# Performance work log

Measured on AMD Instinct MI355X. Metric: run time of the kernel, lower is better.

The kernel has to match this reference:

```python
import jax, jax.numpy as jnp
import numpy as np

RADIUS = 2
B, C, D, H, W = 2, 16, 48, 128, 256
G = 3 * (2 * RADIUS + 1) ** 2  # 75 guidance channels: (2r+1)^2 spatial x 3 depth offsets


def setup_inputs() -> dict:
    key = jax.random.key(0)
    k1, k2 = jax.random.split(key)
    input1 = jax.random.normal(k1, (B, C, D, H, W), dtype=jnp.float32)  # cost volume
    input2 = jax.random.normal(k2, (B, G, H, W), dtype=jnp.float32) * 0.1  # guidance weights
    return {"input1": input1, "input2": input2}


def _lga3d(x, g, r):
    """One pass of local guided aggregation.
    x: [B,C,D,H,W] cost volume; g: [B, 3*(2r+1)^2, H, W] per-pixel weights.
    out[b,c,d,h,w] = sum_{i,j in (2r+1)^2 window, k in {d-1,d,d+1}}
                     g[b, (i*(2r+1)+j)*3+k, h, w] * x[b,c,d+k-1,h+i-r,w+j-r]
    (zero padding out of bounds; weights shared across channels)."""
    w = 2 * r + 1
    bb, cc, dd, hh, ww = x.shape
    # pad depth by 1 on each side, spatial by r on each side
    xp = jnp.pad(x, ((0, 0), (0, 0), (1, 1), (r, r), (r, r)))
    out = jnp.zeros_like(x)
    for i in range(w):          # fixed small window loop (not a data-dim loop)
        for j in range(w):
            for k in range(3):  # depth offsets -1, 0, +1
                idx = (i * w + j) * 3 + k
                patch = jax.lax.dynamic_slice(xp, (0, 0, k, i, j), (bb, cc, dd, hh, ww))
                out = out + g[:, idx][:, None, None, :, :] * patch
    return out


def reference(input1, input2):
    # '2' in LGA3D2: aggregation applied twice with the same guidance
    y = _lga3d(input1, input2, RADIUS)
    return _lga3d(y, input2, RADIUS)
```

## Files before the change

### kernel.cpp

```cpp
#include <hip/hip_runtime.h>
#include <hip/hip_bf16.h>


constexpr int RAD = 2;
constexpr int BB = 2, CC = 16, DD = 48, HH = 128, WW = 256;
constexpr int GG = 75;
constexpr int PLANE = HH * WW;

constexpr int WPT = 4;
constexpr int DPG = 6;
constexpr int NWV = 4;
constexpr int DCHUNK = DPG * NWV;
constexpr int NCH = DD / DCHUNK;
constexpr size_t GPB_UINTS = (size_t)BB * 5 * 9 * PLANE;

using uint = unsigned int;
typedef __attribute__((ext_vector_type(2))) _Float16 half2v;

__device__ __forceinline__ uint pkrtz(float a, float b) {
  return __builtin_bit_cast(uint, __builtin_amdgcn_cvt_pkrtz(a, b));
}
__device__ __forceinline__ float fdot2(uint a, uint b, float c) {
#if __has_builtin(__builtin_amdgcn_fdot2)
  return __builtin_amdgcn_fdot2(__builtin_bit_cast(half2v, a),
                                __builtin_bit_cast(half2v, b), c, false);
#else
  half2v av = __builtin_bit_cast(half2v, a), bv = __builtin_bit_cast(half2v, b);
  return c + (float)av.x * (float)bv.x + (float)av.y * (float)bv.y;
#endif
}
__device__ __forceinline__ uint alignp(uint a, uint b) {
  return __builtin_amdgcn_alignbit(a, b, 16);
}
__device__ __forceinline__ unsigned short f2h(float v) {
  return __builtin_bit_cast(unsigned short, (_Float16)v);
}
__device__ __forceinline__ uint getq(const uint4& v, int q) {
  return q == 0 ? v.x : q == 1 ? v.y : q == 2 ? v.z : v.w;
}

__global__ __launch_bounds__(256) void cvt_f32_f16(const float* __restrict__ x,
                                                   unsigned short* __restrict__ xh,
                                                   int n4) {
  const int stride = gridDim.x * blockDim.x;
  for (int i = blockIdx.x * blockDim.x + threadIdx.x; i < n4; i += stride) {
    const float4 v = *reinterpret_cast<const float4*>(x + (size_t)i * 4);
    uint2 u; u.x = pkrtz(v.x, v.y); u.y = pkrtz(v.z, v.w);
    *reinterpret_cast<uint2*>(xh + (size_t)i * 4) = u;
  }
}

__global__ __launch_bounds__(256) void gpack(const float* __restrict__ g,
                                             uint4* __restrict__ gbuf) {
  const int n = (int)(GPB_UINTS / 4);
  const int stride = gridDim.x * blockDim.x;
  for (int it = blockIdx.x * blockDim.x + threadIdx.x; it < n; it += stride) {
    const int p  = it % 9;
    const int wq = (it / 9) & 63;
    const int h  = (it / (9 * 64)) % HH;
    const int bi = it / (9 * 64 * HH);
    const int i = bi % 5, b = bi / 5;
    const int k = p / 3, jp = p % 3;
    const int chA = (i * 5 + 2 * jp) * 3 + k;
    const float* gb = g + (size_t)b * GG * PLANE + h * WW + 4 * wq;
    const float4 a = *reinterpret_cast<const float4*>(gb + (size_t)chA * PLANE);
    float4 bq = make_float4(0.f, 0.f, 0.f, 0.f);
    if (jp < 2)
      bq = *reinterpret_cast<const float4*>(gb + (size_t)(chA + 3) * PLANE);
    uint4 u;
    u.x = pkrtz(a.x, bq.x); u.y = pkrtz(a.y, bq.y);
    u.z = pkrtz(a.z, bq.z); u.w = pkrtz(a.w, bq.w);
    gbuf[it] = u;
  }
}

template <typename OT, bool PACKED>
__global__ __launch_bounds__(256, 1) void lga_pass(const unsigned short* __restrict__ x,
                                                   const float* __restrict__ g,
                                                   const uint4* __restrict__ gpk,
                                                   OT* __restrict__ out) {
  constexpr int NWG = BB * CC * NCH * HH;
  const int bx = blockIdx.x;
  const int lid = (bx & 7) * (NWG >> 3) + (bx >> 3);
  const int dch = lid % NCH;
  const int h   = (lid / NCH) % HH;
  const int c   = (lid / (NCH * HH)) % CC;
  const int b   =  lid / (NCH * HH * CC);

  const int tid = threadIdx.x;
  const int lane = tid & 63;
  const int dg = tid >> 6;
  const int w0 = lane * WPT;
  const int d0 = dch * DCHUNK + dg * DPG;

  const unsigned short* xb = x + (size_t)(b * CC + c) * DD * PLANE;
  const float* gb = g + (size_t)b * GG * PLANE;

  const int lm1 = ((lane - 1) & 63) * 4;
  const int lp1 = ((lane + 1) & 63) * 4;
  const bool l0 = (lane == 0);
  const bool l63 = (lane == 63);

  float acc[DPG][WPT];
#pragma unroll
  for (int a = 0; a < DPG; ++a)
#pragma unroll
    for (int q = 0; q < WPT; ++q) acc[a][q] = 0.f;

  const int ilo = (h >= RAD) ? 0 : RAD - h;
  const int him = HH - 1 + RAD - h;
  const int ihi = (him < 4) ? him : 4;

  for (int ii = ilo; ii <= ihi; ++ii) {
    const int hr = h + ii - RAD;

    uint4 G[9];
    if constexpr (PACKED) {
      const uint4* gp = gpk + ((size_t)((b * 5 + ii) * HH + h) * 64 + lane) * 9;
#pragma unroll
      for (int p = 0; p < 9; ++p) G[p] = gp[p];
    } else {
#pragma unroll
      for (int k = 0; k < 3; ++k)
#pragma unroll
        for (int jp = 0; jp < 3; ++jp) {
          const int chA = (ii * 5 + 2 * jp) * 3 + k;
          const float4 a = *reinterpret_cast<const float4*>(
              gb + (size_t)chA * PLANE + h * WW + w0);
          float4 bq = make_float4(0.f, 0.f, 0.f, 0.f);
          if (jp < 2)
            bq = *reinterpret_cast<const float4*>(
                gb + (size_t)(chA + 3) * PLANE + h * WW + w0);
          uint4 u;
          u.x = pkrtz(a.x, bq.x); u.y = pkrtz(a.y, bq.y);
          u.z = pkrtz(a.z, bq.z); u.w = pkrtz(a.w, bq.w);
          G[k * 3 + jp] = u;
        }
    }

#pragma unroll
    for (int a = -1; a <= DPG; ++a) {
      bool dok = true;
      if (a == -1)  dok = (d0 > 0);
      if (a == DPG) dok = (d0 + DPG < DD);

      uint2 own = make_uint2(0u, 0u);
      if (dok)
        own = *reinterpret_cast<const uint2*>(
            xb + (size_t)(d0 + a) * PLANE + hr * WW + w0);

      const uint lft = __builtin_amdgcn_ds_bpermute(lm1, (int)own.y);
      const uint rg0 = __builtin_amdgcn_ds_bpermute(lp1, (int)own.x);
      const uint rg1 = __builtin_amdgcn_ds_bpermute(lp1, (int)own.y);
      uint P[9];
      P[0] = l0 ? 0u : lft;
      P[2] = own.x; P[4] = own.y;
      P[6] = l63 ? 0u : rg0;
      P[8] = l63 ? 0u : rg1;
      P[1] = alignp(P[2], P[0]);
      P[3] = alignp(P[4], P[2]);
      P[5] = alignp(P[6], P[4]);
      P[7] = alignp(P[8], P[6]);

#pragma unroll
      for (int k = 0; k < 3; ++k) {
        const int ai = a + 1 - k;
        if (ai < 0 || ai >= DPG) continue;
#pragma unroll
        for (int q = 0; q < WPT; ++q) {
          float t = acc[ai][q];
          t = fdot2(getq(G[k * 3 + 0], q), P[q], t);
          t = fdot2(getq(G[k * 3 + 1], q), P[q + 2], t);
          t = fdot2(getq(G[k * 3 + 2], q), P[q + 4], t);
          acc[ai][q] = t;
        }
      }
    }
  }

  const int obase = d0 * PLANE + h * WW + w0;
  if constexpr (sizeof(OT) == 4) {
    float* ob = (float*)out + (size_t)(b * CC + c) * DD * PLANE;
#pragma unroll
    for (int ai = 0; ai < DPG; ++ai) {
      float4 t; t.x = acc[ai][0]; t.y = acc[ai][1]; t.z = acc[ai][2]; t.w = acc[ai][3];
      *reinterpret_cast<float4*>(ob + obase + ai * PLANE) = t;
    }
  } else {
    unsigned short* ob = (unsigned short*)out + (size_t)(b * CC + c) * DD * PLANE;
#pragma unroll
    for (int ai = 0; ai < DPG; ++ai) {
      ushort4 t; t.x = f2h(acc[ai][0]); t.y = f2h(acc[ai][1]);
      t.z = f2h(acc[ai][2]); t.w = f2h(acc[ai][3]);
      *reinterpret_cast<ushort4*>(ob + obase + ai * PLANE) = t;
    }
  }
}

extern "C" void kernel_launch(void* const* d_in, const int* in_sizes, int n_in,
                              void* d_out, int out_size, void* d_ws, size_t ws_size,
                              hipStream_t stream) {
  const float* x = (const float*)d_in[0];
  const float* g = (const float*)d_in[1];
  float* out = (float*)d_out;

  const size_t elems = (size_t)BB * CC * DD * HH * WW;
  unsigned short* xh = (unsigned short*)d_out;
  unsigned short* y  = (unsigned short*)d_ws;

  cvt_f32_f16<<<2048, 256, 0, stream>>>(x, xh, (int)(elems / 4));

  const dim3 grid(BB * CC * NCH * HH);
  const dim3 block(64 * NWV);

  const size_t need = elems * 2 + GPB_UINTS * 4;
  if (ws_size >= need) {
    uint4* gbuf = (uint4*)((char*)d_ws + elems * 2);
    gpack<<<1440, 256, 0, stream>>>(g, gbuf);
    lga_pass<unsigned short, true><<<grid, block, 0, stream>>>(xh, g, gbuf, y);
    lga_pass<float, true><<<grid, block, 0, stream>>>(y, g, gbuf, out);
  } else {
    lga_pass<unsigned short, false><<<grid, block, 0, stream>>>(xh, g, nullptr, y);
    lga_pass<float, false><<<grid, block, 0, stream>>>(y, g, nullptr, out);
  }
}
```

Measured before the change: 349.6 us.

## Store fp16 volumes in depth/width-padded layout to drop lane shuffles and bounds checks

The fp16 input and intermediate volumes are stored in a padded layout: one zero depth slice on each side and two zero columns left plus six right, giving 264-element rows. Each lane can then load its own 4 columns plus the neighbouring halo with two 8-byte loads. This replaces three ds_bpermute shuffles and the depth-boundary predicates per depth slice. Extra zero_pads kernels write the pads, the conversion and intermediate writes become two 4-byte stores per element group, the buffers grow, and the launch-bounds occupancy hint is relaxed.

```diff
diff --git a/kernel.cpp b/kernel.cpp
--- a/kernel.cpp
+++ b/kernel.cpp
@@ -12,6 +12,10 @@
 constexpr int NWV = 4;
 constexpr int DCHUNK = DPG * NWV;
 constexpr int NCH = DD / DCHUNK;
+constexpr int PW = 264;
+constexpr int DP = DD + 2;
+constexpr size_t PCH = (size_t)DP * HH * PW;
+constexpr size_t PAD_ELEMS = (size_t)BB * CC * PCH;
 constexpr size_t GPB_UINTS = (size_t)BB * 5 * 9 * PLANE;
 
 using uint = unsigned int;
@@ -32,11 +36,23 @@
 __device__ __forceinline__ uint alignp(uint a, uint b) {
   return __builtin_amdgcn_alignbit(a, b, 16);
 }
-__device__ __forceinline__ unsigned short f2h(float v) {
-  return __builtin_bit_cast(unsigned short, (_Float16)v);
-}
 __device__ __forceinline__ uint getq(const uint4& v, int q) {
   return q == 0 ? v.x : q == 1 ? v.y : q == 2 ? v.z : v.w;
+}
+
+__global__ __launch_bounds__(256) void zero_pads(unsigned short* __restrict__ buf) {
+  const int nrows = (int)(BB * CC * DP * HH);
+  const int stride = gridDim.x * blockDim.x;
+  for (int r = blockIdx.x * blockDim.x + threadIdx.x; r < nrows; r += stride) {
+    uint* rowp = reinterpret_cast<uint*>(buf + (size_t)r * PW);
+    const int dpad = (r / HH) % DP;
+    if (dpad == 0 || dpad == DP - 1) {
+      for (int t = 0; t < PW / 2; ++t) rowp[t] = 0u;
+    } else {
+      rowp[0] = 0u;
+      rowp[129] = 0u; rowp[130] = 0u; rowp[131] = 0u;
+    }
+  }
 }
 
 __global__ __launch_bounds__(256) void cvt_f32_f16(const float* __restrict__ x,
@@ -45,8 +61,16 @@
   const int stride = gridDim.x * blockDim.x;
   for (int i = blockIdx.x * blockDim.x + threadIdx.x; i < n4; i += stride) {
     const float4 v = *reinterpret_cast<const float4*>(x + (size_t)i * 4);
-    uint2 u; u.x = pkrtz(v.x, v.y); u.y = pkrtz(v.z, v.w);
-    *reinterpret_cast<uint2*>(xh + (size_t)i * 4) = u;
+    const uint u0 = pkrtz(v.x, v.y);
+    const uint u1 = pkrtz(v.z, v.w);
+    const int w4 = (i & 63) * 4;
+    const int h = (i >> 6) & (HH - 1);
+    const int rest = i >> 13;
+    const int d = rest % DD;
+    const int bc = rest / DD;
+    const size_t hb = ((size_t)(bc * DP + d + 1) * HH + h) * PW + 2 + w4;
+    *reinterpret_cast<uint*>(xh + hb) = u0;
+    *reinterpret_cast<uint*>(xh + hb + 2) = u1;
   }
 }
 
@@ -75,10 +99,10 @@
 }
 
 template <typename OT, bool PACKED>
-__global__ __launch_bounds__(256, 1) void lga_pass(const unsigned short* __restrict__ x,
-                                                   const float* __restrict__ g,
-                                                   const uint4* __restrict__ gpk,
-                                                   OT* __restrict__ out) {
+__global__ __launch_bounds__(256) void lga_pass(const unsigned short* __restrict__ xp,
+                                                const float* __restrict__ g,
+                                                const uint4* __restrict__ gpk,
+                                                OT* __restrict__ out) {
   constexpr int NWG = BB * CC * NCH * HH;
   const int bx = blockIdx.x;
   const int lid = (bx & 7) * (NWG >> 3) + (bx >> 3);
@@ -93,13 +117,9 @@
   const int w0 = lane * WPT;
   const int d0 = dch * DCHUNK + dg * DPG;
 
-  const unsigned short* xb = x + (size_t)(b * CC + c) * DD * PLANE;
+  const int ch = b * CC + c;
+  const unsigned short* xb = xp + (size_t)ch * PCH;
   const float* gb = g + (size_t)b * GG * PLANE;
-
-  const int lm1 = ((lane - 1) & 63) * 4;
-  const int lp1 = ((lane + 1) & 63) * 4;
-  const bool l0 = (lane == 0);
-  const bool l63 = (lane == 63);
 
   float acc[DPG][WPT];
 #pragma unroll
@@ -140,28 +160,15 @@
 
 #pragma unroll
     for (int a = -1; a <= DPG; ++a) {
-      bool dok = true;
-      if (a == -1)  dok = (d0 > 0);
-      if (a == DPG) dok = (d0 + DPG < DD);
-
-      uint2 own = make_uint2(0u, 0u);
-      if (dok)
-        own = *reinterpret_cast<const uint2*>(
-            xb + (size_t)(d0 + a) * PLANE + hr * WW + w0);
-
-      const uint lft = __builtin_amdgcn_ds_bpermute(lm1, (int)own.y);
-      const uint rg0 = __builtin_amdgcn_ds_bpermute(lp1, (int)own.x);
-      const uint rg1 = __builtin_amdgcn_ds_bpermute(lp1, (int)own.y);
-      uint P[9];
-      P[0] = l0 ? 0u : lft;
-      P[2] = own.x; P[4] = own.y;
-      P[6] = l63 ? 0u : rg0;
-      P[8] = l63 ? 0u : rg1;
+      const size_t rh = ((size_t)(d0 + a + 1) * HH + hr) * PW + 4 * lane;
+      const uint2 e01 = *reinterpret_cast<const uint2*>(xb + rh);
+      const uint2 e23 = *reinterpret_cast<const uint2*>(xb + rh + 4);
+      uint P[8];
+      P[0] = e01.x; P[2] = e01.y; P[4] = e23.x; P[6] = e23.y;
       P[1] = alignp(P[2], P[0]);
       P[3] = alignp(P[4], P[2]);
       P[5] = alignp(P[6], P[4]);
-      P[7] = alignp(P[8], P[6]);
-
+      P[7] = alignp(P[6], P[6]);
 #pragma unroll
       for (int k = 0; k < 3; ++k) {
         const int ai = a + 1 - k;
@@ -178,21 +185,21 @@
     }
   }
 
-  const int obase = d0 * PLANE + h * WW + w0;
   if constexpr (sizeof(OT) == 4) {
-    float* ob = (float*)out + (size_t)(b * CC + c) * DD * PLANE;
+    float* ob = (float*)out + (size_t)ch * DD * PLANE;
+    const int obase = d0 * PLANE + h * WW + w0;
 #pragma unroll
     for (int ai = 0; ai < DPG; ++ai) {
       float4 t; t.x = acc[ai][0]; t.y = acc[ai][1]; t.z = acc[ai][2]; t.w = acc[ai][3];
       *reinterpret_cast<float4*>(ob + obase + ai * PLANE) = t;
     }
   } else {
-    unsigned short* ob = (unsigned short*)out + (size_t)(b * CC + c) * DD * PLANE;
+    unsigned short* ob = (unsigned short*)out + (size_t)ch * PCH;
 #pragma unroll
     for (int ai = 0; ai < DPG; ++ai) {
-      ushort4 t; t.x = f2h(acc[ai][0]); t.y = f2h(acc[ai][1]);
-      t.z = f2h(acc[ai][2]); t.w = f2h(acc[ai][3]);
-      *reinterpret_cast<ushort4*>(ob + obase + ai * PLANE) = t;
+      const size_t hb = ((size_t)(d0 + ai + 1) * HH + h) * PW + 2 + w0;
+      *reinterpret_cast<uint*>(ob + hb) = pkrtz(acc[ai][0], acc[ai][1]);
+      *reinterpret_cast<uint*>(ob + hb + 2) = pkrtz(acc[ai][2], acc[ai][3]);
     }
   }
 }
@@ -208,14 +215,16 @@
   unsigned short* xh = (unsigned short*)d_out;
   unsigned short* y  = (unsigned short*)d_ws;
 
+  zero_pads<<<1024, 256, 0, stream>>>(xh);
+  zero_pads<<<1024, 256, 0, stream>>>(y);
   cvt_f32_f16<<<2048, 256, 0, stream>>>(x, xh, (int)(elems / 4));
 
   const dim3 grid(BB * CC * NCH * HH);
   const dim3 block(64 * NWV);
 
-  const size_t need = elems * 2 + GPB_UINTS * 4;
+  const size_t need = PAD_ELEMS * 2 + GPB_UINTS * 4;
   if (ws_size >= need) {
-    uint4* gbuf = (uint4*)((char*)d_ws + elems * 2);
+    uint4* gbuf = (uint4*)((char*)d_ws + PAD_ELEMS * 2);
     gpack<<<1440, 256, 0, stream>>>(g, gbuf);
     lga_pass<unsigned short, true><<<grid, block, 0, stream>>>(xh, g, gbuf, y);
     lga_pass<float, true><<<grid, block, 0, stream>>>(y, g, gbuf, out);
```

New measurement: 450.7 us. 28.9% more time.
